# Performance work log

Hardware: AMD Instinct MI355X
Metric: run time of the kernel (lower is better)

Reference implementation:

```python
import jax, jax.numpy as jnp
import numpy as np

V, E, H = 4996, 64, 64  # vocab, embed dim, GRU units per direction
B, S = 128, 512


def _gru_scan(xw, mask, U, b_r):
    """Masked GRU (Keras reset_after=True semantics).
    xw:   [S, B, 3H] precomputed input projections (x@W + b_input)
    mask: [S, B, 1] bool; masked steps carry previous state (Keras masking).
    U:    [H, 3H] recurrent kernel, b_r: [3H] recurrent bias.
    Returns per-step hidden states [S, B, H].
    """
    def step(h, inp):
        xw_t, m = inp
        rec = h @ U + b_r                                   # [B, 3H]
        z = jax.nn.sigmoid(xw_t[:, :H] + rec[:, :H])        # update gate
        r = jax.nn.sigmoid(xw_t[:, H:2*H] + rec[:, H:2*H])  # reset gate
        hh = jnp.tanh(xw_t[:, 2*H:] + r * rec[:, 2*H:])     # candidate
        h_new = z * h + (1.0 - z) * hh
        h = jnp.where(m, h_new, h)                          # skip masked steps
        return h, h

    h0 = jnp.zeros((xw.shape[1], H), xw.dtype)
    _, ys = jax.lax.scan(step, h0, (xw, mask))
    return ys


def setup_inputs() -> dict:
    key = jax.random.key(0)
    ks = jax.random.split(key, 12)
    sc = 0.1
    inp = {
        "inputs": jax.random.randint(ks[0], (B, S), 0, V),
        "emb": jax.random.normal(ks[1], (V, E), jnp.float32) * sc,
        "Wf": jax.random.normal(ks[2], (E, 3 * H), jnp.float32) * sc,
        "Uf": jax.random.normal(ks[3], (H, 3 * H), jnp.float32) * sc,
        "bif": jnp.zeros((3 * H,), jnp.float32),
        "brf": jnp.zeros((3 * H,), jnp.float32),
        "Wb": jax.random.normal(ks[4], (E, 3 * H), jnp.float32) * sc,
        "Ub": jax.random.normal(ks[5], (H, 3 * H), jnp.float32) * sc,
        "bib": jnp.zeros((3 * H,), jnp.float32),
        "brb": jnp.zeros((3 * H,), jnp.float32),
        "w1": jax.random.normal(ks[6], (2 * H, 1), jnp.float32) * sc,
        "b1": jnp.zeros((1,), jnp.float32),
        "w2": jax.random.normal(ks[7], (2 * H, 1), jnp.float32) * sc,
        "b2": jnp.zeros((1,), jnp.float32),
    }
    return inp


def reference(inputs, emb, Wf, Uf, bif, brf, Wb, Ub, bib, brb, w1, b1, w2, b2):
    mask = (inputs != 0)                       # [B, S] mask_zero semantics
    x = emb[inputs]                            # [B, S, E]
    xt = jnp.swapaxes(x, 0, 1)                 # [S, B, E] time-major
    m = jnp.swapaxes(mask, 0, 1)[:, :, None]   # [S, B, 1]

    # forward direction
    fwd = _gru_scan(xt @ Wf + bif, m, Uf, brf)                 # [S, B, H]
    # backward direction: reverse time, scan, reverse back
    bwd = _gru_scan((xt @ Wb + bib)[::-1], m[::-1], Ub, brb)[::-1]

    gru_out = jnp.swapaxes(jnp.concatenate([fwd, bwd], axis=-1), 0, 1)  # [B, S, 2H]
    x1 = jax.nn.sigmoid(gru_out @ w1 + b1)     # [B, S, 1]
    x2 = jax.nn.sigmoid(gru_out @ w2 + b2)     # [B, S, 1]
    return x1, x2, gru_out
```

## Files before the change

kernel.cpp:

```cpp
#include <hip/hip_runtime.h>
#include <hip/hip_bf16.h>
#include <hip/hip_fp16.h>

#define B_  128
#define S_  512
#define H_  64
#define E_  64
#define G3  192
#define V_  4996
#define VCHUNK 32
#define CHUNK  16
#define NCHUNK (S_ / CHUNK)
#define STOK  (S_ + CHUNK)

typedef float f32x4 __attribute__((ext_vector_type(4)));
typedef unsigned int u32;
typedef u32 u32x4 __attribute__((ext_vector_type(4)));
typedef _Float16 f16;
typedef f16 f16x2 __attribute__((ext_vector_type(2)));

__device__ __forceinline__ float fast_rcp(float x) {
#if __has_builtin(__builtin_amdgcn_rcpf)
    return __builtin_amdgcn_rcpf(x);
#else
    return 1.0f / x;
#endif
}
__device__ __forceinline__ float fast_exp(float x) {
#if __has_builtin(__builtin_amdgcn_exp2f)
    return __builtin_amdgcn_exp2f(x * 1.44269504f);
#else
    return __expf(x);
#endif
}
__device__ __forceinline__ float sigmoidf_(float x) {
    return fast_rcp(1.0f + fast_exp(-x));
}
__device__ __forceinline__ float tanh_fast(float x) {
    return 1.0f - 2.0f * fast_rcp(1.0f + fast_exp(2.0f * x));
}

__device__ __forceinline__ float fdot2_(u32 a, u32 b, float c) {
#if __has_builtin(__builtin_amdgcn_fdot2)
    return __builtin_amdgcn_fdot2(__builtin_bit_cast(f16x2, a),
                                  __builtin_bit_cast(f16x2, b), c, false);
#else
    const f16x2 av = __builtin_bit_cast(f16x2, a);
    const f16x2 bv = __builtin_bit_cast(f16x2, b);
    return fmaf((float)av.x, (float)bv.x, fmaf((float)av.y, (float)bv.y, c));
#endif
}

__global__ __launch_bounds__(192) void proj_kernel(
    const float* __restrict__ emb,
    const float* __restrict__ Wf, const float* __restrict__ bif,
    const float* __restrict__ Wb, const float* __restrict__ bib,
    float* __restrict__ proj)
{
    const int dir = blockIdx.y;
    const float* W  = dir ? Wb  : Wf;
    const float* bi = dir ? bib : bif;
    const int v0 = blockIdx.x * VCHUNK;
    const int j  = threadIdx.x;
    const int nrows = min(VCHUNK, V_ - v0);

    __shared__ __align__(16) float s_e[VCHUNK * E_];
    for (int i = j; i < nrows * E_; i += 192) s_e[i] = emb[(size_t)v0 * E_ + i];

    float wcol[E_];
    #pragma unroll
    for (int e = 0; e < E_; ++e) wcol[e] = W[e * G3 + j];
    const float bij = bi[j];
    __syncthreads();

    for (int r = 0; r < nrows; ++r) {
        const float4* x4 = (const float4*)(s_e + r * E_);
        float a0 = 0.f, a1 = 0.f, a2 = 0.f, a3 = 0.f;
        #pragma unroll
        for (int e4 = 0; e4 < 16; e4 += 4) {
            float4 h0 = x4[e4], h1 = x4[e4+1], h2 = x4[e4+2], h3 = x4[e4+3];
            a0 = fmaf(h0.x, wcol[4*e4+ 0], a0); a0 = fmaf(h0.y, wcol[4*e4+ 1], a0);
            a0 = fmaf(h0.z, wcol[4*e4+ 2], a0); a0 = fmaf(h0.w, wcol[4*e4+ 3], a0);
            a1 = fmaf(h1.x, wcol[4*e4+ 4], a1); a1 = fmaf(h1.y, wcol[4*e4+ 5], a1);
            a1 = fmaf(h1.z, wcol[4*e4+ 6], a1); a1 = fmaf(h1.w, wcol[4*e4+ 7], a1);
            a2 = fmaf(h2.x, wcol[4*e4+ 8], a2); a2 = fmaf(h2.y, wcol[4*e4+ 9], a2);
            a2 = fmaf(h2.z, wcol[4*e4+10], a2); a2 = fmaf(h2.w, wcol[4*e4+11], a2);
            a3 = fmaf(h3.x, wcol[4*e4+12], a3); a3 = fmaf(h3.y, wcol[4*e4+13], a3);
            a3 = fmaf(h3.z, wcol[4*e4+14], a3); a3 = fmaf(h3.w, wcol[4*e4+15], a3);
        }
        proj[((size_t)dir * V_ + v0 + r) * G3 + j] = ((a0 + a1) + (a2 + a3)) + bij;
    }
}

__global__ void upack_kernel(const float* __restrict__ Uf,
                             const float* __restrict__ Ub,
                             u32* __restrict__ Uh)
{
    const int dir = blockIdx.x;
    const float* U = dir ? Ub : Uf;
    u32* o = Uh + (size_t)dir * G3 * 32;
    for (int k = threadIdx.x; k < G3 * 32; k += blockDim.x) {
        const int j = k >> 5, kk = k & 31;
        f16x2 p;
        p.x = (f16)U[(2 * kk    ) * G3 + j];
        p.y = (f16)U[(2 * kk + 1) * G3 + j];
        o[(size_t)j * 32 + kk] = __builtin_bit_cast(u32, p);
    }
}

__global__ __launch_bounds__(64)
__attribute__((amdgpu_waves_per_eu(1, 1)))
void gru_scan9(
    const int*   __restrict__ inputs,
    const float* __restrict__ proj,
    const u32*   __restrict__ Uh,
    const float* __restrict__ brf, const float* __restrict__ brb,
    float* __restrict__ gru_out)
{
    const int b   = blockIdx.x >> 1;
    const int dir = blockIdx.x & 1;
    const int u   = threadIdx.x;

    const float* eproj = proj + (size_t)dir * V_ * G3;
    const float* br    = dir ? brb : brf;

    __shared__ __align__(16) int   s_tok[STOK];
    __shared__ __align__(16) f16   s_h[H_];
    __shared__ __align__(16) float s_xw[2][CHUNK * G3];

    for (int t = u; t < S_; t += 64)
        s_tok[t] = inputs[b * S_ + (dir ? (S_ - 1 - t) : t)];
    for (int t = S_ + u; t < STOK; t += 64) s_tok[t] = 0;
    s_h[u] = (f16)0.0f;
    __builtin_amdgcn_wave_barrier();

    u32x4 wz[8], wr[8], wc[8];
    {
        const u32x4* pz = (const u32x4*)(Uh + ((size_t)dir * G3 + u      ) * 32);
        const u32x4* pr = (const u32x4*)(Uh + ((size_t)dir * G3 + u + 64 ) * 32);
        const u32x4* pc = (const u32x4*)(Uh + ((size_t)dir * G3 + u + 128) * 32);
        #pragma unroll
        for (int k = 0; k < 8; ++k) { wz[k] = pz[k]; wr[k] = pr[k]; wc[k] = pc[k]; }
        #pragma unroll
        for (int k = 0; k < 8; ++k) {
            asm volatile("" : "+v"(wz[k]));
            asm volatile("" : "+v"(wr[k]));
            asm volatile("" : "+v"(wc[k]));
        }
    }
    const float br0 = br[u], br1 = br[u + 64], br2 = br[u + 128];
    float hprev = 0.0f;

    f32x4 ld[12];
    auto stage_issue = [&](int baseStep) {
        #pragma unroll
        for (int i = 0; i < 12; ++i) {
            const int idx = i * 64 + u;
            const int row = idx / 48;
            const int off = idx - row * 48;
            const int tk  = s_tok[baseStep + row];
            ld[i] = *(const f32x4*)(eproj + (size_t)tk * G3 + off * 4);
        }
    };
    auto stage_write = [&](int nbuf) {
        #pragma unroll
        for (int i = 0; i < 12; ++i) {
            const int idx = i * 64 + u;
            *(f32x4*)(&s_xw[nbuf][idx * 4]) = ld[i];
        }
    };

    stage_issue(0);
    stage_write(0);
    __builtin_amdgcn_wave_barrier();

    float* outb = gru_out + (size_t)b * S_ * (2 * H_) + dir * H_ + u;

    for (int c = 0; c < NCHUNK; ++c) {
        const int buf = c & 1;
        stage_issue((c + 1) * CHUNK);

        #pragma unroll 1
        for (int t0 = 0; t0 < CHUNK; ++t0) {
            const int t = c * CHUNK + t0;

            const int   tok = s_tok[t];
            const float x0  = s_xw[buf][t0 * G3 + u];
            const float x1  = s_xw[buf][t0 * G3 + u + 64];
            const float x2  = s_xw[buf][t0 * G3 + u + 128];

            const u32x4* h8 = (const u32x4*)s_h;
            float az[4] = {0,0,0,0}, ar_[4] = {0,0,0,0}, ac_[4] = {0,0,0,0};
            #pragma unroll
            for (int k = 0; k < 8; ++k) {
                const u32x4 hv = h8[k];
                const u32x4 vz = wz[k], vr = wr[k], vc = wc[k];
                az[0]  = fdot2_(hv.x, vz.x, az[0]);
                az[1]  = fdot2_(hv.y, vz.y, az[1]);
                az[2]  = fdot2_(hv.z, vz.z, az[2]);
                az[3]  = fdot2_(hv.w, vz.w, az[3]);
                ar_[0] = fdot2_(hv.x, vr.x, ar_[0]);
                ar_[1] = fdot2_(hv.y, vr.y, ar_[1]);
                ar_[2] = fdot2_(hv.z, vr.z, ar_[2]);
                ar_[3] = fdot2_(hv.w, vr.w, ar_[3]);
                ac_[0] = fdot2_(hv.x, vc.x, ac_[0]);
                ac_[1] = fdot2_(hv.y, vc.y, ac_[1]);
                ac_[2] = fdot2_(hv.z, vc.z, ac_[2]);
                ac_[3] = fdot2_(hv.w, vc.w, ac_[3]);
            }
            const float d0 = ((az[0]  + az[1])  + (az[2]  + az[3]))  + br0;
            const float d1 = ((ar_[0] + ar_[1]) + (ar_[2] + ar_[3])) + br1;
            const float d2 = ((ac_[0] + ac_[1]) + (ac_[2] + ac_[3])) + br2;

            const float z    = sigmoidf_(x0 + d0);
            const float r    = sigmoidf_(x1 + d1);
            const float hh   = tanh_fast(fmaf(r, d2, x2));
            const float hnew = fmaf(z, hprev - hh, hh);
            const float res  = (tok != 0) ? hnew : hprev;
            hprev = res;

            s_h[u] = (f16)res;
            __builtin_amdgcn_wave_barrier();

            const int tt = dir ? (S_ - 1 - t) : t;
            outb[(size_t)tt * (2 * H_)] = res;
        }

        stage_write(buf ^ 1);
        __builtin_amdgcn_wave_barrier();
    }
}

__global__ __launch_bounds__(256) void head_kernel(
    const float* __restrict__ gru,
    const float* __restrict__ w1, const float* __restrict__ b1,
    const float* __restrict__ w2, const float* __restrict__ b2,
    float* __restrict__ x1, float* __restrict__ x2)
{
    __shared__ __align__(16) float s_w1[2 * H_];
    __shared__ __align__(16) float s_w2[2 * H_];
    const int tid = threadIdx.x;
    if (tid < 2 * H_)      s_w1[tid]          = w1[tid];
    else                   s_w2[tid - 2 * H_] = w2[tid - 2 * H_];
    __syncthreads();

    const int i = blockIdx.x * 256 + tid;
    const float4* g4 = (const float4*)(gru + (size_t)i * (2 * H_));
    float a1 = b1[0], a2 = b2[0];
    #pragma unroll
    for (int k = 0; k < (2 * H_) / 4; ++k) {
        const float4 v  = g4[k];
        const float4 q1 = ((const float4*)s_w1)[k];
        const float4 q2 = ((const float4*)s_w2)[k];
        a1 += v.x * q1.x + v.y * q1.y + v.z * q1.z + v.w * q1.w;
        a2 += v.x * q2.x + v.y * q2.y + v.z * q2.z + v.w * q2.w;
    }
    x1[i] = 1.0f / (1.0f + __expf(-a1));
    x2[i] = 1.0f / (1.0f + __expf(-a2));
}

extern "C" void kernel_launch(void* const* d_in, const int* in_sizes, int n_in,
                              void* d_out, int out_size, void* d_ws, size_t ws_size,
                              hipStream_t stream) {
    (void)in_sizes; (void)n_in; (void)ws_size; (void)out_size;

    const int*   inputs = (const int*)  d_in[0];
    const float* emb    = (const float*)d_in[1];
    const float* Wf     = (const float*)d_in[2];
    const float* Uf     = (const float*)d_in[3];
    const float* bif    = (const float*)d_in[4];
    const float* brf    = (const float*)d_in[5];
    const float* Wb     = (const float*)d_in[6];
    const float* Ub     = (const float*)d_in[7];
    const float* bib    = (const float*)d_in[8];
    const float* brb    = (const float*)d_in[9];
    const float* w1     = (const float*)d_in[10];
    const float* b1     = (const float*)d_in[11];
    const float* w2     = (const float*)d_in[12];
    const float* b2     = (const float*)d_in[13];

    float* out = (float*)d_out;
    float* x1  = out;
    float* x2  = out + (size_t)B_ * S_;
    float* gru = out + (size_t)2 * B_ * S_;

    float* proj = (float*)d_ws;
    u32*   Uh   = (u32*)(proj + (size_t)2 * V_ * G3);

    proj_kernel<<<dim3((V_ + VCHUNK - 1) / VCHUNK, 2), 192, 0, stream>>>(
        emb, Wf, bif, Wb, bib, proj);
    upack_kernel<<<2, 256, 0, stream>>>(Uf, Ub, Uh);

    gru_scan9<<<B_ * 2, 64, 0, stream>>>(inputs, proj, Uh, brf, brb, gru);

    head_kernel<<<(B_ * S_) / 256, 256, 0, stream>>>(gru, w1, b1, w2, b2, x1, x2);
}
```

Baseline: 235.8 us.

## Process two batch rows per wave in GRU scan to share recurrent weights

Each single-wave block now advances two batch sequences in the same direction, reusing the register-resident recurrent weights and interleaving two independent dependency chains per timestep. The grid is halved, and the staging chunk is cut from 16 to 8 steps so shared-memory and register use for staged projections stays similar. This trades fewer active CUs for more instruction-level parallelism per step, which may lengthen each step's serial latency.

New measurement: 391.9 us. 1.66x slower.

```diff
diff --git a/kernel.cpp b/kernel.cpp
--- a/kernel.cpp
+++ b/kernel.cpp
@@ -9,7 +9,7 @@
 #define G3  192
 #define V_  4996
 #define VCHUNK 32
-#define CHUNK  16
+#define CHUNK  8
 #define NCHUNK (S_ / CHUNK)
 #define STOK  (S_ + CHUNK)
 
@@ -110,28 +110,33 @@
 
 __global__ __launch_bounds__(64)
 __attribute__((amdgpu_waves_per_eu(1, 1)))
-void gru_scan9(
+void gru_scan10(
     const int*   __restrict__ inputs,
     const float* __restrict__ proj,
     const u32*   __restrict__ Uh,
     const float* __restrict__ brf, const float* __restrict__ brb,
     float* __restrict__ gru_out)
 {
-    const int b   = blockIdx.x >> 1;
-    const int dir = blockIdx.x & 1;
-    const int u   = threadIdx.x;
+    const int dir  = blockIdx.x & 1;
+    const int pair = blockIdx.x >> 1;
+    const int b0   = pair * 2, b1 = pair * 2 + 1;
+    const int u    = threadIdx.x;
 
     const float* eproj = proj + (size_t)dir * V_ * G3;
     const float* br    = dir ? brb : brf;
 
-    __shared__ __align__(16) int   s_tok[STOK];
-    __shared__ __align__(16) f16   s_h[H_];
-    __shared__ __align__(16) float s_xw[2][CHUNK * G3];
-
-    for (int t = u; t < S_; t += 64)
-        s_tok[t] = inputs[b * S_ + (dir ? (S_ - 1 - t) : t)];
-    for (int t = S_ + u; t < STOK; t += 64) s_tok[t] = 0;
-    s_h[u] = (f16)0.0f;
+    __shared__ __align__(16) int   s_tok[2][STOK];
+    __shared__ __align__(16) f16   s_h[2][H_];
+    __shared__ __align__(16) float s_xw[2][2][CHUNK * G3];
+
+    for (int t = u; t < S_; t += 64) {
+        const int tt = dir ? (S_ - 1 - t) : t;
+        s_tok[0][t] = inputs[b0 * S_ + tt];
+        s_tok[1][t] = inputs[b1 * S_ + tt];
+    }
+    for (int t = S_ + u; t < STOK; t += 64) { s_tok[0][t] = 0; s_tok[1][t] = 0; }
+    s_h[0][u] = (f16)0.0f;
+    s_h[1][u] = (f16)0.0f;
     __builtin_amdgcn_wave_barrier();
 
     u32x4 wz[8], wr[8], wc[8];
@@ -149,24 +154,25 @@
         }
     }
     const float br0 = br[u], br1 = br[u + 64], br2 = br[u + 128];
-    float hprev = 0.0f;
-
-    f32x4 ld[12];
+    float hprev0 = 0.0f, hprev1 = 0.0f;
+
+    f32x4 ld0[6], ld1[6];
     auto stage_issue = [&](int baseStep) {
         #pragma unroll
-        for (int i = 0; i < 12; ++i) {
+        for (int i = 0; i < 6; ++i) {
             const int idx = i * 64 + u;
             const int row = idx / 48;
             const int off = idx - row * 48;
-            const int tk  = s_tok[baseStep + row];
-            ld[i] = *(const f32x4*)(eproj + (size_t)tk * G3 + off * 4);
+            ld0[i] = *(const f32x4*)(eproj + (size_t)s_tok[0][baseStep + row] * G3 + off * 4);
+            ld1[i] = *(const f32x4*)(eproj + (size_t)s_tok[1][baseStep + row] * G3 + off * 4);
         }
     };
     auto stage_write = [&](int nbuf) {
         #pragma unroll
-        for (int i = 0; i < 12; ++i) {
+        for (int i = 0; i < 6; ++i) {
             const int idx = i * 64 + u;
-            *(f32x4*)(&s_xw[nbuf][idx * 4]) = ld[i];
+            *(f32x4*)(&s_xw[nbuf][0][idx * 4]) = ld0[i];
+            *(f32x4*)(&s_xw[nbuf][1][idx * 4]) = ld1[i];
         }
     };
 
@@ -174,7 +180,8 @@
     stage_write(0);
     __builtin_amdgcn_wave_barrier();
 
-    float* outb = gru_out + (size_t)b * S_ * (2 * H_) + dir * H_ + u;
+    float* outb0 = gru_out + (size_t)b0 * S_ * (2 * H_) + dir * H_ + u;
+    float* outb1 = gru_out + (size_t)b1 * S_ * (2 * H_) + dir * H_ + u;
 
     for (int c = 0; c < NCHUNK; ++c) {
         const int buf = c & 1;
@@ -184,46 +191,81 @@
         for (int t0 = 0; t0 < CHUNK; ++t0) {
             const int t = c * CHUNK + t0;
 
-            const int   tok = s_tok[t];
-            const float x0  = s_xw[buf][t0 * G3 + u];
-            const float x1  = s_xw[buf][t0 * G3 + u + 64];
-            const float x2  = s_xw[buf][t0 * G3 + u + 128];
-
-            const u32x4* h8 = (const u32x4*)s_h;
-            float az[4] = {0,0,0,0}, ar_[4] = {0,0,0,0}, ac_[4] = {0,0,0,0};
+            const int tok0 = s_tok[0][t];
+            const int tok1 = s_tok[1][t];
+            const float x00 = s_xw[buf][0][t0 * G3 + u];
+            const float x01 = s_xw[buf][0][t0 * G3 + u + 64];
+            const float x02 = s_xw[buf][0][t0 * G3 + u + 128];
+            const float x10 = s_xw[buf][1][t0 * G3 + u];
+            const float x11 = s_xw[buf][1][t0 * G3 + u + 64];
+            const float x12 = s_xw[buf][1][t0 * G3 + u + 128];
+
+            const u32x4* h0p = (const u32x4*)s_h[0];
+            const u32x4* h1p = (const u32x4*)s_h[1];
+            u32x4 h0v[8], h1v[8];
+            #pragma unroll
+            for (int k = 0; k < 8; ++k) h0v[k] = h0p[k];
+            #pragma unroll
+            for (int k = 0; k < 8; ++k) h1v[k] = h1p[k];
+
+            float a0z[4] = {0,0,0,0}, a0r[4] = {0,0,0,0}, a0c[4] = {0,0,0,0};
+            float a1z[4] = {0,0,0,0}, a1r[4] = {0,0,0,0}, a1c[4] = {0,0,0,0};
             #pragma unroll
             for (int k = 0; k < 8; ++k) {
-                const u32x4 hv = h8[k];
+                const u32x4 v0 = h0v[k], v1 = h1v[k];
                 const u32x4 vz = wz[k], vr = wr[k], vc = wc[k];
-                az[0]  = fdot2_(hv.x, vz.x, az[0]);
-                az[1]  = fdot2_(hv.y, vz.y, az[1]);
-                az[2]  = fdot2_(hv.z, vz.z, az[2]);
-                az[3]  = fdot2_(hv.w, vz.w, az[3]);
-                ar_[0] = fdot2_(hv.x, vr.x, ar_[0]);
-                ar_[1] = fdot2_(hv.y, vr.y, ar_[1]);
-                ar_[2] = fdot2_(hv.z, vr.z, ar_[2]);
-                ar_[3] = fdot2_(hv.w, vr.w, ar_[3]);
-                ac_[0] = fdot2_(hv.x, vc.x, ac_[0]);
-                ac_[1] = fdot2_(hv.y, vc.y, ac_[1]);
-                ac_[2] = fdot2_(hv.z, vc.z, ac_[2]);
-                ac_[3] = fdot2_(hv.w, vc.w, ac_[3]);
+                a0z[0] = fdot2_(v0.x, vz.x, a0z[0]);
+                a0z[1] = fdot2_(v0.y, vz.y, a0z[1]);
+                a0z[2] = fdot2_(v0.z, vz.z, a0z[2]);
+                a0z[3] = fdot2_(v0.w, vz.w, a0z[3]);
+                a1z[0] = fdot2_(v1.x, vz.x, a1z[0]);
+                a1z[1] = fdot2_(v1.y, vz.y, a1z[1]);
+                a1z[2] = fdot2_(v1.z, vz.z, a1z[2]);
+                a1z[3] = fdot2_(v1.w, vz.w, a1z[3]);
+                a0r[0] = fdot2_(v0.x, vr.x, a0r[0]);
+                a0r[1] = fdot2_(v0.y, vr.y, a0r[1]);
+                a0r[2] = fdot2_(v0.z, vr.z, a0r[2]);
+                a0r[3] = fdot2_(v0.w, vr.w, a0r[3]);
+                a1r[0] = fdot2_(v1.x, vr.x, a1r[0]);
+                a1r[1] = fdot2_(v1.y, vr.y, a1r[1]);
+                a1r[2] = fdot2_(v1.z, vr.z, a1r[2]);
+                a1r[3] = fdot2_(v1.w, vr.w, a1r[3]);
+                a0c[0] = fdot2_(v0.x, vc.x, a0c[0]);
+                a0c[1] = fdot2_(v0.y, vc.y, a0c[1]);
+                a0c[2] = fdot2_(v0.z, vc.z, a0c[2]);
+                a0c[3] = fdot2_(v0.w, vc.w, a0c[3]);
+                a1c[0] = fdot2_(v1.x, vc.x, a1c[0]);
+                a1c[1] = fdot2_(v1.y, vc.y, a1c[1]);
+                a1c[2] = fdot2_(v1.z, vc.z, a1c[2]);
+                a1c[3] = fdot2_(v1.w, vc.w, a1c[3]);
             }
-            const float d0 = ((az[0]  + az[1])  + (az[2]  + az[3]))  + br0;
-            const float d1 = ((ar_[0] + ar_[1]) + (ar_[2] + ar_[3])) + br1;
-            const float d2 = ((ac_[0] + ac_[1]) + (ac_[2] + ac_[3])) + br2;
-
-            const float z    = sigmoidf_(x0 + d0);
-            const float r    = sigmoidf_(x1 + d1);
-            const float hh   = tanh_fast(fmaf(r, d2, x2));
-            const float hnew = fmaf(z, hprev - hh, hh);
-            const float res  = (tok != 0) ? hnew : hprev;
-            hprev = res;
-
-            s_h[u] = (f16)res;
+            const float d00 = ((a0z[0]+a0z[1]) + (a0z[2]+a0z[3])) + br0;
+            const float d01 = ((a0r[0]+a0r[1]) + (a0r[2]+a0r[3])) + br1;
+            const float d02 = ((a0c[0]+a0c[1]) + (a0c[2]+a0c[3])) + br2;
+            const float d10 = ((a1z[0]+a1z[1]) + (a1z[2]+a1z[3])) + br0;
+            const float d11 = ((a1r[0]+a1r[1]) + (a1r[2]+a1r[3])) + br1;
+            const float d12 = ((a1c[0]+a1c[1]) + (a1c[2]+a1c[3])) + br2;
+
+            const float z0 = sigmoidf_(x00 + d00);
+            const float z1 = sigmoidf_(x10 + d10);
+            const float r0 = sigmoidf_(x01 + d01);
+            const float r1 = sigmoidf_(x11 + d11);
+            const float hh0 = tanh_fast(fmaf(r0, d02, x02));
+            const float hh1 = tanh_fast(fmaf(r1, d12, x12));
+            const float hn0 = fmaf(z0, hprev0 - hh0, hh0);
+            const float hn1 = fmaf(z1, hprev1 - hh1, hh1);
+            const float res0 = (tok0 != 0) ? hn0 : hprev0;
+            const float res1 = (tok1 != 0) ? hn1 : hprev1;
+            hprev0 = res0;
+            hprev1 = res1;
+
+            s_h[0][u] = (f16)res0;
+            s_h[1][u] = (f16)res1;
             __builtin_amdgcn_wave_barrier();
 
             const int tt = dir ? (S_ - 1 - t) : t;
-            outb[(size_t)tt * (2 * H_)] = res;
+            outb0[(size_t)tt * (2 * H_)] = res0;
+            outb1[(size_t)tt * (2 * H_)] = res1;
         }
 
         stage_write(buf ^ 1);
@@ -291,7 +333,7 @@
         emb, Wf, bif, Wb, bib, proj);
     upack_kernel<<<2, 256, 0, stream>>>(Uf, Ub, Uh);
 
-    gru_scan9<<<B_ * 2, 64, 0, stream>>>(inputs, proj, Uh, brf, brb, gru);
+    gru_scan10<<<B_, 64, 0, stream>>>(inputs, proj, Uh, brf, brb, gru);
 
     head_kernel<<<(B_ * S_) / 256, 256, 0, stream>>>(gru, w1, b1, w2, b2, x1, x2);
 }
```
